# Kernel optimization log

Measured on AMD Instinct MI355X. Metric: run time of the kernel, lower is better.

Reference implementation:

```python
import jax, jax.numpy as jnp
import numpy as np
from jax import lax

B, H, W = 32, 40, 256
FREQ = 40            # freq_num
WIND = 0.5           # wind_size (seconds)
KF = 5               # input_filter_kernel (odd -> 'same' length)
CNN_OUT = 64 * 36 * 252  # out_channels[-1] * (H-4) * (W-4)


def setup_inputs() -> dict:
    key = jax.random.key(0)
    ks = jax.random.split(key, 9)
    return {
        "inputs": jax.random.normal(ks[0], (B, 1, H, W), jnp.float32),
        "w0": jax.random.normal(ks[1], (32, 1, 3, 3), jnp.float32) * 0.1,
        "b0": jax.random.normal(ks[2], (32,), jnp.float32) * 0.05,
        "w1": jax.random.normal(ks[3], (64, 32, 3, 3), jnp.float32) * 0.05,
        "b1": jax.random.normal(ks[4], (64,), jnp.float32) * 0.05,
        "wf": jax.random.normal(ks[5], (1, 1, 1, KF), jnp.float32) * 0.2,
        "bf": jax.random.normal(ks[6], (1,), jnp.float32) * 0.05,
        "wr": jax.random.normal(ks[7], (FREQ, CNN_OUT), jnp.float32) * 1e-3,
        "br": jax.random.normal(ks[8], (FREQ,), jnp.float32) * 0.05,
    }


def _conv2d(x, w, padding):
    return lax.conv_general_dilated(
        x, w, window_strides=(1, 1), padding=padding,
        dimension_numbers=("NCHW", "OIHW", "NCHW"))


def reference(inputs, w0, b0, w1, b1, wf, bf, wr, br):
    b, _, h, w_len = inputs.shape
    # input_filter: Conv1d(1,1,KF, padding=KF//2) applied independently per
    # frequency row -> equivalent to a 2D conv with a (1,KF) kernel.
    p = KF // 2
    feats = _conv2d(inputs, wf, [(0, 0), (p, p)]) + bf[None, :, None, None]  # [B,1,H,W]

    # conv stack with ReLU
    x = jax.nn.relu(_conv2d(inputs, w0, "VALID") + b0[None, :, None, None])
    x = jax.nn.relu(_conv2d(x, w1, "VALID") + b1[None, :, None, None])

    gates = jax.nn.sigmoid(x.reshape(b, -1) @ wr.T + br)

    fs = (1.0 / WIND) * jnp.linspace(1.0, FREQ, FREQ)          # [FREQ]
    wtd_mean_mod = jnp.mean(gates * fs[None, :])               # scalar

    # Fused modulation transform: instead of the per-frequency python loop
    # with materialized [B,H,W] broadcasts, compute sin/cos bases [FREQ,W]
    # and reduce over time with a single einsum each.
    t = jnp.linspace(0.0, WIND, w_len)                          # [W]
    phase = (2.0 * np.pi) * fs[:, None] * t[None, :]            # [FREQ,W]
    f0 = feats[:, 0]                                            # [B,H,W]
    inv_w = jnp.float32(1.0 / w_len)
    sins = jnp.einsum("fw,bhw->bfh", jnp.sin(phase), f0) * inv_w  # mean over W
    coss = jnp.einsum("fw,bhw->bfh", jnp.cos(phase), f0) * inv_w
    mag = jnp.sqrt(sins * sins + coss * coss)                   # [B,FREQ,H]
    mods = (mag * gates[:, :, None]).reshape(b, FREQ * h)       # cat over freq, dim=1
    return mods, wtd_mean_mod
```

## Files before the change

### kernel.cpp

```cpp
#include <hip/hip_runtime.h>
#include <hip/hip_bf16.h>
#include <math.h>

#define BB   32
#define HH   40
#define WW   256
#define NF   40
#define H1N  36
#define W1N  252
#define KCNN 580608
#define KT   256
#define NBLK2 1134

typedef __attribute__((ext_vector_type(8))) short bf16x8;
typedef __attribute__((ext_vector_type(4))) float f32x4;

static __device__ __forceinline__ unsigned short f2bf(float v) {
    __hip_bfloat16 h = __float2bfloat16(v);
    return *(unsigned short*)&h;
}

__global__ void k0_prep(const float* __restrict__ w1, unsigned short* __restrict__ w1c,
                        float* __restrict__ gacc8, float* __restrict__ sintab,
                        float* __restrict__ costab, float* __restrict__ out) {
    int o = blockIdx.x * 256 + threadIdx.x;
    int c0  = o & 31;
    int c1  = (o >> 5) & 63;
    int tap = o >> 11;
    w1c[o] = f2bf(w1[(c1 * 32 + c0) * 9 + tap]);
    if (o < 10240) {
        int f = o >> 8, w = o & 255;
        float ph = 6.283185307179586f * (float)(f + 1) * (1.0f / 255.0f) * (float)w;
        sintab[o] = sinf(ph);
        costab[o] = cosf(ph);
        gacc8[o] = 0.0f;
    }
    if (o == 0) out[51200] = 0.0f;
}

__global__ __launch_bounds__(256) void k1_conv(
        const float* __restrict__ inp, const float* __restrict__ w0,
        const float* __restrict__ b0, const unsigned short* __restrict__ w1c,
        const float* __restrict__ b1, unsigned short* __restrict__ xbf) {
    __shared__ __align__(16) char smem[33856];
    float* ins = (float*)smem;
    unsigned short* y0T = (unsigned short*)(smem + 2176);
    unsigned short* stg = (unsigned short*)smem;

    const int jt = blockIdx.x;
    const int it = blockIdx.y;
    const int b  = blockIdx.z;
    const int i0 = it * 4;
    const int j0 = jt * 64;
    const int tid = threadIdx.x;

    if (tid < 136) {
        int r  = tid / 17, c4 = tid - r * 17;
        float4 v = {0.f, 0.f, 0.f, 0.f};
        if (jt < 3 || c4 < 16)
            v = *(const float4*)(inp + (b * HH + i0 + r) * WW + j0 + c4 * 4);
        *(float4*)(ins + r * 68 + c4 * 4) = v;
    }
    __syncthreads();

    {
        const int c0 = tid & 31;
        const int pg = tid >> 5;
        if (pg < 6) {
            float wreg[9];
            #pragma unroll
            for (int k = 0; k < 9; ++k) wreg[k] = w0[c0 * 9 + k];
            const float bias = b0[c0];
            const float4* rp0 = (const float4*)(ins + (pg    ) * 68);
            const float4* rp1 = (const float4*)(ins + (pg + 1) * 68);
            const float4* rp2 = (const float4*)(ins + (pg + 2) * 68);
            unsigned short* yrow = y0T + pg * 66 * 40 + c0;
            float4 a0 = rp0[0], a1 = rp1[0], a2 = rp2[0];
            #pragma unroll 2
            for (int ch = 0; ch < 8; ++ch) {
                float4 b0v = rp0[2 * ch + 1], c0v = rp0[2 * ch + 2];
                float4 b1v = rp1[2 * ch + 1], c1v = rp1[2 * ch + 2];
                float4 b2v = rp2[2 * ch + 1], c2v = rp2[2 * ch + 2];
                float r0[12] = {a0.x,a0.y,a0.z,a0.w,b0v.x,b0v.y,b0v.z,b0v.w,c0v.x,c0v.y,c0v.z,c0v.w};
                float r1[12] = {a1.x,a1.y,a1.z,a1.w,b1v.x,b1v.y,b1v.z,b1v.w,c1v.x,c1v.y,c1v.z,c1v.w};
                float r2[12] = {a2.x,a2.y,a2.z,a2.w,b2v.x,b2v.y,b2v.z,b2v.w,c2v.x,c2v.y,c2v.z,c2v.w};
                #pragma unroll
                for (int t = 0; t < 8; ++t) {
                    int col = ch * 8 + t;
                    float a = bias;
                    #pragma unroll
                    for (int kj = 0; kj < 3; ++kj) {
                        a = fmaf(r0[t + kj], wreg[kj],     a);
                        a = fmaf(r1[t + kj], wreg[3 + kj], a);
                        a = fmaf(r2[t + kj], wreg[6 + kj], a);
                    }
                    float v = (j0 + col < 254) ? fmaxf(a, 0.0f) : 0.0f;
                    yrow[col * 40] = f2bf(v);
                }
                a0 = c0v; a1 = c1v; a2 = c2v;
            }
            {
                float t0[4] = {a0.x, a0.y, a0.z, a0.w};
                float t1[4] = {a1.x, a1.y, a1.z, a1.w};
                float t2[4] = {a2.x, a2.y, a2.z, a2.w};
                #pragma unroll
                for (int t = 0; t < 2; ++t) {
                    int col = 64 + t;
                    float a = bias;
                    #pragma unroll
                    for (int kj = 0; kj < 3; ++kj) {
                        a = fmaf(t0[t + kj], wreg[kj],     a);
                        a = fmaf(t1[t + kj], wreg[3 + kj], a);
                        a = fmaf(t2[t + kj], wreg[6 + kj], a);
                    }
                    float v = (j0 + col < 254) ? fmaxf(a, 0.0f) : 0.0f;
                    yrow[col * 40] = f2bf(v);
                }
            }
        }
    }
    __syncthreads();

    const int w    = tid >> 6;
    const int lane = tid & 63;
    const int l15  = lane & 15;
    const int quad = lane >> 4;

    float biasr[4][4];
    #pragma unroll
    for (int mt = 0; mt < 4; ++mt)
        #pragma unroll
        for (int rg = 0; rg < 4; ++rg)
            biasr[mt][rg] = b1[mt * 16 + quad * 4 + rg];

    f32x4 acc[4][4];
    #pragma unroll
    for (int mt = 0; mt < 4; ++mt)
        #pragma unroll
        for (int nt = 0; nt < 4; ++nt)
            acc[mt][nt] = (f32x4){0.f, 0.f, 0.f, 0.f};

    #pragma unroll
    for (int ki = 0; ki < 3; ++ki) {
        #pragma unroll
        for (int kj = 0; kj < 3; ++kj) {
            const int tap = ki * 3 + kj;
            bf16x8 af[4], bfr[4];
            #pragma unroll
            for (int mt = 0; mt < 4; ++mt)
                af[mt] = *(const bf16x8*)(w1c + ((tap * 64 + mt * 16 + l15) * 32 + quad * 8));
            #pragma unroll
            for (int nt = 0; nt < 4; ++nt)
                bfr[nt] = *(const bf16x8*)(y0T + (((w + ki) * 66 + nt * 16 + l15 + kj) * 40 + quad * 8));
            #pragma unroll
            for (int mt = 0; mt < 4; ++mt)
                #pragma unroll
                for (int nt = 0; nt < 4; ++nt)
                    acc[mt][nt] = __builtin_amdgcn_mfma_f32_16x16x32_bf16(
                        af[mt], bfr[nt], acc[mt][nt], 0, 0, 0);
        }
    }

    __syncthreads();
    #pragma unroll
    for (int mt = 0; mt < 4; ++mt)
        #pragma unroll
        for (int nt = 0; nt < 4; ++nt)
            #pragma unroll
            for (int rg = 0; rg < 4; ++rg) {
                int c1 = mt * 16 + quad * 4 + rg;
                int j  = nt * 16 + l15;
                int jr = (j + (((c1 >> 2) & 3) << 4)) & 63;
                float v = fmaxf(acc[mt][nt][rg] + biasr[mt][rg], 0.0f);
                stg[(c1 * 4 + w) * 64 + jr] = f2bf(v);
            }
    __syncthreads();

    const int limit = (j0 + 64 <= W1N) ? 64 : (W1N - j0);
    for (int it2 = 0; it2 < 16; ++it2) {
        int cc = it2 * 256 + tid;
        int e  = cc * 4;
        int c1 = e >> 8;
        int w2 = (e >> 6) & 3;
        int jb = e & 63;
        if (jb < limit) {
            int jr = (jb + (((c1 >> 2) & 3) << 4)) & 63;
            *(uint2*)(xbf + (size_t)b * KCNN + (c1 * H1N + i0 + w2) * W1N + j0 + jb) =
                *(const uint2*)(stg + (c1 * 4 + w2) * 64 + jr);
        }
    }
}

__global__ __launch_bounds__(256) void k2_gemm(
        const unsigned short* __restrict__ xbf, const float* __restrict__ wr,
        float* __restrict__ gacc8) {
    __shared__ __align__(16) char smem[42240];
    unsigned short* lx = (unsigned short*)smem;
    unsigned short* lw = (unsigned short*)(smem + 16896);
    float (*red)[32][41] = (float (*)[32][41])smem;

    const int tid  = threadIdx.x;
    const int wv   = tid >> 6;
    const int lane = tid & 63;
    const int l15  = lane & 15;
    const int quad = lane >> 4;

    for (int i = tid; i < 264; i += 256) {
        int row = 40 + i / 33, seg = i % 33;
        *(bf16x8*)(lw + row * 264 + seg * 8) = (bf16x8){0,0,0,0,0,0,0,0};
    }

    f32x4 acc[2][3];
    #pragma unroll
    for (int mt = 0; mt < 2; ++mt)
        #pragma unroll
        for (int nt = 0; nt < 3; ++nt)
            acc[mt][nt] = (f32x4){0.f, 0.f, 0.f, 0.f};

    for (int it = 0; it < 2; ++it) {
        const size_t kt = (size_t)(blockIdx.x + it * NBLK2) * KT;
        __syncthreads();

        for (int i = tid; i < 1024; i += 256) {
            int row = i >> 5, seg = i & 31;
            *(bf16x8*)(lx + row * 264 + seg * 8) =
                *(const bf16x8*)(xbf + (size_t)row * KCNN + kt + seg * 8);
        }
        for (int i = tid; i < 2560; i += 256) {
            int row = i >> 6, seg = i & 63;
            float4 v = *(const float4*)(wr + (size_t)row * KCNN + kt + seg * 4);
            ushort4 p = { f2bf(v.x), f2bf(v.y), f2bf(v.z), f2bf(v.w) };
            *(ushort4*)(lw + row * 264 + seg * 4) = p;
        }
        __syncthreads();

        #pragma unroll
        for (int c = 0; c < 2; ++c) {
            const int lk = wv * 64 + c * 32;
            bf16x8 af[2], bfr[3];
            af[0] = *(const bf16x8*)(lx + (l15     ) * 264 + lk + quad * 8);
            af[1] = *(const bf16x8*)(lx + (16 + l15) * 264 + lk + quad * 8);
            #pragma unroll
            for (int nt = 0; nt < 3; ++nt)
                bfr[nt] = *(const bf16x8*)(lw + (nt * 16 + l15) * 264 + lk + quad * 8);
            #pragma unroll
            for (int nt = 0; nt < 3; ++nt) {
                acc[0][nt] = __builtin_amdgcn_mfma_f32_16x16x32_bf16(af[0], bfr[nt], acc[0][nt], 0, 0, 0);
                acc[1][nt] = __builtin_amdgcn_mfma_f32_16x16x32_bf16(af[1], bfr[nt], acc[1][nt], 0, 0, 0);
            }
        }
    }

    __syncthreads();
    #pragma unroll
    for (int mt = 0; mt < 2; ++mt)
        #pragma unroll
        for (int nt = 0; nt < 3; ++nt)
            #pragma unroll
            for (int rg = 0; rg < 4; ++rg) {
                int bb = mt * 16 + quad * 4 + rg;
                int ff = nt * 16 + l15;
                if (ff < NF) red[wv][bb][ff] = acc[mt][nt][rg];
            }
    __syncthreads();
    float* myg = gacc8 + (size_t)(blockIdx.x & 7) * 1280;
    for (int p = tid; p < 1280; p += 256) {
        int bb = p / 40, ff = p - bb * 40;
        float s = 0.0f;
        #pragma unroll
        for (int w = 0; w < 4; ++w) s += red[w][bb][ff];
        atomicAdd(myg + p, s);
    }
}

__global__ __launch_bounds__(320) void k4_mods(
        const float* __restrict__ inp, const float* __restrict__ sintab,
        const float* __restrict__ costab, const float* __restrict__ wf,
        const float* __restrict__ bfp, const float* __restrict__ gacc8,
        const float* __restrict__ br, float* __restrict__ out) {
    const int f = blockIdx.x, b = blockIdx.y;
    const int tid = threadIdx.x;
    const int h  = tid >> 3;
    const int wl = tid & 7;

    float s = 0.0f;
    #pragma unroll
    for (int r = 0; r < 8; ++r) s += gacc8[r * 1280 + b * 40 + f];
    const float g = 1.0f / (1.0f + __expf(-(s + br[f])));
    if (tid == 0)
        atomicAdd(out + 51200, g * (2.0f * (float)(f + 1)) * (1.0f / 1280.0f));

    float wfv[5];
    #pragma unroll
    for (int t = 0; t < 5; ++t) wfv[t] = wf[t];
    const float bias = bfp[0];
    const float* row  = inp + (b * HH + h) * WW;
    const float* srow = sintab + f * 256;
    const float* crow = costab + f * 256;
    float sa = 0.0f, ca = 0.0f;
    for (int m = 0; m < 32; ++m) {
        int w = wl + 8 * m;
        float feat = bias;
        #pragma unroll
        for (int d = -2; d <= 2; ++d) {
            int wc = w + d;
            if (wc >= 0 && wc < WW) feat = fmaf(row[wc], wfv[d + 2], feat);
        }
        sa = fmaf(srow[w], feat, sa);
        ca = fmaf(crow[w], feat, ca);
    }
    #pragma unroll
    for (int off = 4; off >= 1; off >>= 1) {
        sa += __shfl_xor(sa, off, 8);
        ca += __shfl_xor(ca, off, 8);
    }
    if (wl == 0) {
        float mag = sqrtf(sa * sa + ca * ca) * (1.0f / 256.0f);
        out[b * 1600 + f * 40 + h] = mag * g;
    }
}

extern "C" void kernel_launch(void* const* d_in, const int* in_sizes, int n_in,
                              void* d_out, int out_size, void* d_ws, size_t ws_size,
                              hipStream_t stream) {
    const float* inp = (const float*)d_in[0];
    const float* w0  = (const float*)d_in[1];
    const float* b0  = (const float*)d_in[2];
    const float* w1  = (const float*)d_in[3];
    const float* b1  = (const float*)d_in[4];
    const float* wf  = (const float*)d_in[5];
    const float* bf_ = (const float*)d_in[6];
    const float* wr  = (const float*)d_in[7];
    const float* br  = (const float*)d_in[8];
    float* out = (float*)d_out;

    char* ws = (char*)d_ws;
    unsigned short* xbf = (unsigned short*)ws;
    unsigned short* w1c = (unsigned short*)(ws + 37158912);
    float* gacc8  = (float*)(ws + 37195776);
    float* sintab = (float*)(ws + 37236736);
    float* costab = (float*)(ws + 37277696);

    k0_prep<<<72, 256, 0, stream>>>(w1, w1c, gacc8, sintab, costab, out);
    k1_conv<<<dim3(4, 9, 32), 256, 0, stream>>>(inp, w0, b0, w1c, b1, xbf);
    k2_gemm<<<NBLK2, 256, 0, stream>>>(xbf, wr, gacc8);
    k4_mods<<<dim3(40, 32), 320, 0, stream>>>(inp, sintab, costab, wf, bf_, gacc8, br, out);
}
```

Before: 240.9 us.

## Load GEMM tiles directly into LDS and convert wr to bf16 at fragment load

The split-K regression GEMM now stages the x and wr tiles with global_load_lds (direct global-to-LDS loads) instead of register round-trips. wr stays fp32 in LDS and is converted to bf16 while building the MFMA B fragment. K tile size drops from 256 to 128 with four contiguous tiles per block, which shrinks LDS use from about 42 KB to 32 KB. This is meant to cut VGPR traffic and load latency and to raise occupancy. In exchange it drops the padded LDS row stride, so bank conflicts are possible, and it adds per-iteration conversion work.

```diff
diff --git a/kernel.cpp b/kernel.cpp
--- a/kernel.cpp
+++ b/kernel.cpp
@@ -9,7 +9,8 @@
 #define H1N  36
 #define W1N  252
 #define KCNN 580608
-#define KT   256
+#define KT2  128
+#define NT2  4
 #define NBLK2 1134
 
 typedef __attribute__((ext_vector_type(8))) short bf16x8;
@@ -18,6 +19,21 @@
 static __device__ __forceinline__ unsigned short f2bf(float v) {
     __hip_bfloat16 h = __float2bfloat16(v);
     return *(unsigned short*)&h;
+}
+
+static __device__ __forceinline__ bf16x8 packbf(float4 lo, float4 hi) {
+    bf16x8 r;
+    r[0] = (short)f2bf(lo.x); r[1] = (short)f2bf(lo.y);
+    r[2] = (short)f2bf(lo.z); r[3] = (short)f2bf(lo.w);
+    r[4] = (short)f2bf(hi.x); r[5] = (short)f2bf(hi.y);
+    r[6] = (short)f2bf(hi.z); r[7] = (short)f2bf(hi.w);
+    return r;
+}
+
+static __device__ __forceinline__ void gll16(const void* g, void* l) {
+    __builtin_amdgcn_global_load_lds(
+        (const __attribute__((address_space(1))) void*)g,
+        (__attribute__((address_space(3))) void*)l, 16, 0, 0);
 }
 
 __global__ void k0_prep(const float* __restrict__ w1, unsigned short* __restrict__ w1c,
@@ -194,9 +210,9 @@
 __global__ __launch_bounds__(256) void k2_gemm(
         const unsigned short* __restrict__ xbf, const float* __restrict__ wr,
         float* __restrict__ gacc8) {
-    __shared__ __align__(16) char smem[42240];
+    __shared__ __align__(16) char smem[32768];
     unsigned short* lx = (unsigned short*)smem;
-    unsigned short* lw = (unsigned short*)(smem + 16896);
+    float* lwf = (float*)(smem + 8192);
     float (*red)[32][41] = (float (*)[32][41])smem;
 
     const int tid  = threadIdx.x;
@@ -204,11 +220,10 @@
     const int lane = tid & 63;
     const int l15  = lane & 15;
     const int quad = lane >> 4;
-
-    for (int i = tid; i < 264; i += 256) {
-        int row = 40 + i / 33, seg = i % 33;
-        *(bf16x8*)(lw + row * 264 + seg * 8) = (bf16x8){0,0,0,0,0,0,0,0};
-    }
+    const int gx = lane >> 4, ix = lane & 15;
+    const int gw = lane >> 5, iw = lane & 31;
+
+    *(float4*)((char*)lwf + 40 * 512 + tid * 16) = (float4){0.f, 0.f, 0.f, 0.f};
 
     f32x4 acc[2][3];
     #pragma unroll
@@ -217,37 +232,35 @@
         for (int nt = 0; nt < 3; ++nt)
             acc[mt][nt] = (f32x4){0.f, 0.f, 0.f, 0.f};
 
-    for (int it = 0; it < 2; ++it) {
-        const size_t kt = (size_t)(blockIdx.x + it * NBLK2) * KT;
+    for (int it = 0; it < NT2; ++it) {
+        const size_t kt = (size_t)(blockIdx.x * NT2 + it) * KT2;
         __syncthreads();
 
-        for (int i = tid; i < 1024; i += 256) {
-            int row = i >> 5, seg = i & 31;
-            *(bf16x8*)(lx + row * 264 + seg * 8) =
-                *(const bf16x8*)(xbf + (size_t)row * KCNN + kt + seg * 8);
-        }
-        for (int i = tid; i < 2560; i += 256) {
-            int row = i >> 6, seg = i & 63;
-            float4 v = *(const float4*)(wr + (size_t)row * KCNN + kt + seg * 4);
-            ushort4 p = { f2bf(v.x), f2bf(v.y), f2bf(v.z), f2bf(v.w) };
-            *(ushort4*)(lw + row * 264 + seg * 4) = p;
+        #pragma unroll
+        for (int jj = 0; jj < 2; ++jj) {
+            const int j = wv * 2 + jj;
+            gll16(xbf + (size_t)(4 * j + gx) * KCNN + kt + ix * 8,
+                  (char*)smem + j * 1024);
+        }
+        #pragma unroll
+        for (int jj = 0; jj < 5; ++jj) {
+            const int j = wv * 5 + jj;
+            gll16(wr + (size_t)(2 * j + gw) * KCNN + kt + iw * 4,
+                  (char*)smem + 8192 + j * 1024);
         }
         __syncthreads();
 
-        #pragma unroll
-        for (int c = 0; c < 2; ++c) {
-            const int lk = wv * 64 + c * 32;
-            bf16x8 af[2], bfr[3];
-            af[0] = *(const bf16x8*)(lx + (l15     ) * 264 + lk + quad * 8);
-            af[1] = *(const bf16x8*)(lx + (16 + l15) * 264 + lk + quad * 8);
-            #pragma unroll
-            for (int nt = 0; nt < 3; ++nt)
-                bfr[nt] = *(const bf16x8*)(lw + (nt * 16 + l15) * 264 + lk + quad * 8);
-            #pragma unroll
-            for (int nt = 0; nt < 3; ++nt) {
-                acc[0][nt] = __builtin_amdgcn_mfma_f32_16x16x32_bf16(af[0], bfr[nt], acc[0][nt], 0, 0, 0);
-                acc[1][nt] = __builtin_amdgcn_mfma_f32_16x16x32_bf16(af[1], bfr[nt], acc[1][nt], 0, 0, 0);
-            }
+        const int lk = wv * 32;
+        bf16x8 af0 = *(const bf16x8*)(lx + l15 * 128 + lk + quad * 8);
+        bf16x8 af1 = *(const bf16x8*)(lx + (16 + l15) * 128 + lk + quad * 8);
+        #pragma unroll
+        for (int nt = 0; nt < 3; ++nt) {
+            const float* bp = lwf + (nt * 16 + l15) * 128 + lk + quad * 8;
+            float4 lo = *(const float4*)bp;
+            float4 hi = *(const float4*)(bp + 4);
+            bf16x8 bfrag = packbf(lo, hi);
+            acc[0][nt] = __builtin_amdgcn_mfma_f32_16x16x32_bf16(af0, bfrag, acc[0][nt], 0, 0, 0);
+            acc[1][nt] = __builtin_amdgcn_mfma_f32_16x16x32_bf16(af1, bfrag, acc[1][nt], 0, 0, 0);
         }
     }
 
```

Measured after the change: 232.9 us. 3.3% less time.
